# Kernel optimization log

Measured on AMD Instinct MI355X. Metric: run time of the kernel, lower is better.

The kernel has to match this reference:

```python
import jax, jax.numpy as jnp
import numpy as np


def setup_inputs() -> dict:
    key = jax.random.key(0)
    x = jax.random.normal(key, (8, 50, 64, 64, 32), dtype=jnp.float32)
    return {
        "x": x,
        "hp_alif_d": jnp.float32(0.9),      # membrane decay
        "hp_alif_adp": jnp.float32(0.9),    # threshold adaptation decay
        "hp_alif_beta": jnp.float32(1.8),   # adaptation increment per spike
        "hp_alpha": jnp.float32(2.0),       # surrogate-gradient sharpness
    }


def reference(x, hp_alif_d, hp_alif_adp, hp_alif_beta, hp_alpha):
    # x: [B, T, H, W, C] -> time-major [T, B, H, W, C]
    x_seq = jnp.moveaxis(x, 1, 0)

    def scan_fn(carry, x_t):
        v, theta, prev_s = carry
        theta_next = theta * hp_alif_adp + prev_s * hp_alif_beta
        v_next = v * hp_alif_d + x_t
        vth_t = 0.5 + theta_next  # adaptive threshold
        s = jnp.where(v_next - vth_t > 0, 1.0, 0.0).astype(x_t.dtype)
        v_next = v_next - s * vth_t  # soft reset by threshold
        return (v_next, theta_next, s), s

    z = jnp.zeros_like(x_seq[0])
    _, spikes = jax.lax.scan(scan_fn, (z, z, z), x_seq)
    return jnp.moveaxis(spikes, 0, 1)  # back to [B, T, H, W, C]
```

## Files before the change

### kernel.cpp

```cpp
#include <hip/hip_runtime.h>


constexpr int B_  = 8;
constexpr int T_  = 50;
constexpr int HWC = 64 * 64 * 32;
constexpr int NV  = HWC / 4;

__global__ __launch_bounds__(256) void alif_fwd_kernel(
    const float4* __restrict__ x, float4* __restrict__ out,
    const float* __restrict__ pd, const float* __restrict__ padp,
    const float* __restrict__ pbeta)
{
    const int tid = blockIdx.x * blockDim.x + threadIdx.x;
    const int b   = tid / NV;
    const int p   = tid % NV;

    const float dcy  = *pd;
    const float adp  = *padp;
    const float beta = *pbeta;

    const float4* xp = x   + (size_t)b * T_ * NV + p;
    float4*       op = out + (size_t)b * T_ * NV + p;

    float v[4]  = {0.f, 0.f, 0.f, 0.f};
    float th[4] = {0.f, 0.f, 0.f, 0.f};
    float ps[4] = {0.f, 0.f, 0.f, 0.f};

    for (int t = 0; t < T_; ++t) {
        float4 xv = xp[(size_t)t * NV];
        float xs[4] = {xv.x, xv.y, xv.z, xv.w};
        float s[4];
        #pragma unroll
        for (int i = 0; i < 4; ++i) {
            th[i] = __fadd_rn(__fmul_rn(th[i], adp), __fmul_rn(ps[i], beta));
            v[i]  = __fadd_rn(__fmul_rn(v[i], dcy), xs[i]);
            float vth = __fadd_rn(0.5f, th[i]);
            s[i]  = (__fsub_rn(v[i], vth) > 0.0f) ? 1.0f : 0.0f;
            v[i]  = __fsub_rn(v[i], __fmul_rn(s[i], vth));
            ps[i] = s[i];
        }
        float4 ov;
        ov.x = s[0]; ov.y = s[1]; ov.z = s[2]; ov.w = s[3];
        op[(size_t)t * NV] = ov;
    }
}

extern "C" void kernel_launch(void* const* d_in, const int* in_sizes, int n_in,
                              void* d_out, int out_size, void* d_ws, size_t ws_size,
                              hipStream_t stream) {
    const float4* x    = (const float4*)d_in[0];
    const float*  pd   = (const float*)d_in[1];
    const float*  padp = (const float*)d_in[2];
    const float*  pbet = (const float*)d_in[3];
    float4* out = (float4*)d_out;

    const int total_threads = B_ * NV;
    const int block = 256;
    const int grid  = total_threads / block;

    alif_fwd_kernel<<<grid, block, 0, stream>>>(x, out, pd, padp, pbet);
}
```

Measured before the change: 355.4 us.

## Software-prefetch input timesteps in chunks with nontemporal loads and stores

Restructures the time loop into chunks of five steps, loading the next chunk's inputs into registers while the current chunk is computed, so more memory requests are in flight per thread. All global loads and stores also become nontemporal to avoid polluting the cache with streaming data. The cost is extra registers for the double-buffered chunk, which could lower occupancy.

```diff
diff --git a/kernel.cpp b/kernel.cpp
--- a/kernel.cpp
+++ b/kernel.cpp
@@ -1,13 +1,16 @@
 #include <hip/hip_runtime.h>
 
+
+typedef float v4f __attribute__((ext_vector_type(4)));
 
 constexpr int B_  = 8;
 constexpr int T_  = 50;
 constexpr int HWC = 64 * 64 * 32;
 constexpr int NV  = HWC / 4;
+constexpr int K_  = 5;
 
 __global__ __launch_bounds__(256) void alif_fwd_kernel(
-    const float4* __restrict__ x, float4* __restrict__ out,
+    const v4f* __restrict__ x, v4f* __restrict__ out,
     const float* __restrict__ pd, const float* __restrict__ padp,
     const float* __restrict__ pbeta)
 {
@@ -19,40 +22,56 @@
     const float adp  = *padp;
     const float beta = *pbeta;
 
-    const float4* xp = x   + (size_t)b * T_ * NV + p;
-    float4*       op = out + (size_t)b * T_ * NV + p;
+    const v4f* xp = x   + (size_t)b * T_ * NV + p;
+    v4f*       op = out + (size_t)b * T_ * NV + p;
 
     float v[4]  = {0.f, 0.f, 0.f, 0.f};
     float th[4] = {0.f, 0.f, 0.f, 0.f};
     float ps[4] = {0.f, 0.f, 0.f, 0.f};
 
-    for (int t = 0; t < T_; ++t) {
-        float4 xv = xp[(size_t)t * NV];
-        float xs[4] = {xv.x, xv.y, xv.z, xv.w};
-        float s[4];
+    v4f cur[K_];
+    #pragma unroll
+    for (int k = 0; k < K_; ++k)
+        cur[k] = __builtin_nontemporal_load(xp + (size_t)k * NV);
+
+    for (int t0 = 0; t0 < T_; t0 += K_) {
+        v4f nxt[K_];
+        if (t0 + K_ < T_) {
+            #pragma unroll
+            for (int k = 0; k < K_; ++k)
+                nxt[k] = __builtin_nontemporal_load(xp + (size_t)(t0 + K_ + k) * NV);
+        }
+
         #pragma unroll
-        for (int i = 0; i < 4; ++i) {
-            th[i] = __fadd_rn(__fmul_rn(th[i], adp), __fmul_rn(ps[i], beta));
-            v[i]  = __fadd_rn(__fmul_rn(v[i], dcy), xs[i]);
-            float vth = __fadd_rn(0.5f, th[i]);
-            s[i]  = (__fsub_rn(v[i], vth) > 0.0f) ? 1.0f : 0.0f;
-            v[i]  = __fsub_rn(v[i], __fmul_rn(s[i], vth));
-            ps[i] = s[i];
+        for (int k = 0; k < K_; ++k) {
+            float s[4];
+            #pragma unroll
+            for (int i = 0; i < 4; ++i) {
+                const float xi = cur[k][i];
+                th[i] = __fadd_rn(__fmul_rn(th[i], adp), __fmul_rn(ps[i], beta));
+                v[i]  = __fadd_rn(__fmul_rn(v[i], dcy), xi);
+                float vth = __fadd_rn(0.5f, th[i]);
+                s[i]  = (__fsub_rn(v[i], vth) > 0.0f) ? 1.0f : 0.0f;
+                v[i]  = __fsub_rn(v[i], __fmul_rn(s[i], vth));
+                ps[i] = s[i];
+            }
+            v4f ov = {s[0], s[1], s[2], s[3]};
+            __builtin_nontemporal_store(ov, op + (size_t)(t0 + k) * NV);
         }
-        float4 ov;
-        ov.x = s[0]; ov.y = s[1]; ov.z = s[2]; ov.w = s[3];
-        op[(size_t)t * NV] = ov;
+
+        #pragma unroll
+        for (int k = 0; k < K_; ++k) cur[k] = nxt[k];
     }
 }
 
 extern "C" void kernel_launch(void* const* d_in, const int* in_sizes, int n_in,
                               void* d_out, int out_size, void* d_ws, size_t ws_size,
                               hipStream_t stream) {
-    const float4* x    = (const float4*)d_in[0];
-    const float*  pd   = (const float*)d_in[1];
-    const float*  padp = (const float*)d_in[2];
-    const float*  pbet = (const float*)d_in[3];
-    float4* out = (float4*)d_out;
+    const v4f*   x    = (const v4f*)d_in[0];
+    const float* pd   = (const float*)d_in[1];
+    const float* padp = (const float*)d_in[2];
+    const float* pbet = (const float*)d_in[3];
+    v4f* out = (v4f*)d_out;
 
     const int total_threads = B_ * NV;
     const int block = 256;
```

New measurement: 339.8 us. -4.4%, faster.
